# Performance work log

Hardware: AMD Instinct MI355X
Metric: run time of the kernel (lower is better)

The kernel has to match this reference:

```python
import jax, jax.numpy as jnp
import numpy as np

S = 4096            # num tokens (single causal sequence)
HID = 1024          # hidden_size
NH = 16             # num query heads
NKV = 4             # num kv heads
HD = 64             # head_dim
THETA = 10000.0
Q_SIZE = NH * HD
KV_SIZE = NKV * HD


def setup_inputs() -> dict:
    key = jax.random.key(0)
    k1, k2, k3 = jax.random.split(key, 3)
    return {
        "positions": jnp.arange(S, dtype=jnp.int32),
        "hidden_states": jax.random.normal(k1, (S, 2 * HID), dtype=jnp.float32),
        "w_qkv": jax.random.normal(k2, (Q_SIZE + 2 * KV_SIZE, 2 * HID), dtype=jnp.float32) * 0.02,
        "w_o": jax.random.normal(k3, (HID, Q_SIZE), dtype=jnp.float32) * 0.02,
    }


def _rope(x, positions):
    # x: [S, H, HD]; neox-style rotate-half RoPE
    half = HD // 2
    inv_freq = 1.0 / (THETA ** (jnp.arange(0, half, dtype=jnp.float32) / half))
    freqs = positions.astype(jnp.float32)[:, None] * inv_freq  # [S, half]
    cos = jnp.cos(freqs)[:, None, :]  # [S, 1, half]
    sin = jnp.sin(freqs)[:, None, :]
    x1, x2 = x[..., :half], x[..., half:]
    return jnp.concatenate([x1 * cos - x2 * sin, x2 * cos + x1 * sin], axis=-1)


def reference(positions, hidden_states, w_qkv, w_o):
    qkv = hidden_states @ w_qkv.T  # [S, Q_SIZE + 2*KV_SIZE]
    q = qkv[:, :Q_SIZE].reshape(S, NH, HD)
    k = qkv[:, Q_SIZE:Q_SIZE + KV_SIZE].reshape(S, NKV, HD)
    v = qkv[:, Q_SIZE + KV_SIZE:].reshape(S, NKV, HD)
    q = _rope(q, positions)
    k = _rope(k, positions)
    # GQA: group query heads over kv heads
    g = NH // NKV
    qg = q.reshape(S, NKV, g, HD)
    scale = HD ** -0.5
    scores = jnp.einsum("qhgd,thd->hgqt", qg, k) * scale  # [NKV, g, S, S]
    causal = positions[:, None] >= positions[None, :]      # [S, S]
    scores = jnp.where(causal[None, None], scores, jnp.finfo(scores.dtype).min)
    probs = jax.nn.softmax(scores, axis=-1)
    o = jnp.einsum("hgqt,thd->qhgd", probs, v).reshape(S, Q_SIZE)
    return o @ w_o.T  # [S, HID]
```

## Files before the change

kernel.cpp:

```cpp
#include <hip/hip_runtime.h>
#include <math.h>

#define S_LEN   4096
#define NHEADS  16
#define NKVH    4
#define HDIM    64
#define QKV_N   1536
#define HID2    2048
#define OUT_N   1024

typedef __attribute__((ext_vector_type(8))) __bf16 bf16x8;
typedef __attribute__((ext_vector_type(4))) __bf16 bf16x4;
typedef __attribute__((ext_vector_type(4))) float  f32x4;
typedef __attribute__((ext_vector_type(16))) float f32x16;
typedef __attribute__((ext_vector_type(4))) unsigned int u32x4;

#define GL_LDS16(gaddr, laddr)                                                  \
  __builtin_amdgcn_global_load_lds(                                             \
      (const __attribute__((address_space(1))) unsigned int*)(gaddr),           \
      (__attribute__((address_space(3))) unsigned int*)(laddr), 16, 0, 0)

__device__ __forceinline__ unsigned cvt_pk_bf16(float lo, float hi) {
  unsigned r;
  asm("v_cvt_pk_bf16_f32 %0, %1, %2" : "=v"(r) : "v"(lo), "v"(hi));
  return r;
}

__global__ __launch_bounds__(256) void cvt_all(const float* __restrict__ hid,
                                               const float* __restrict__ wq,
                                               const float* __restrict__ wo,
                                               __bf16* __restrict__ hid_bf,
                                               __bf16* __restrict__ wq_bf,
                                               __bf16* __restrict__ wo_bf) {
  const int n1 = S_LEN * HID2;
  const int n2 = QKV_N * HID2;
  int i = (blockIdx.x * blockDim.x + threadIdx.x) * 8;
  const float* src; __bf16* dst; int off;
  if (i < n1)           { src = hid; dst = hid_bf; off = i; }
  else if (i < n1 + n2) { src = wq;  dst = wq_bf;  off = i - n1; }
  else                  { src = wo;  dst = wo_bf;  off = i - n1 - n2; }
  float4 a = *(const float4*)(src + off);
  float4 b = *(const float4*)(src + off + 4);
  bf16x8 o = {(__bf16)a.x,(__bf16)a.y,(__bf16)a.z,(__bf16)a.w,
              (__bf16)b.x,(__bf16)b.y,(__bf16)b.z,(__bf16)b.w};
  *(bf16x8*)(dst + off) = o;
}

__global__ __launch_bounds__(256) void rope_table(const int* __restrict__ positions,
                                                  float* __restrict__ ct,
                                                  float* __restrict__ st) {
  int i = blockIdx.x * blockDim.x + threadIdx.x;
  int s = i >> 5, d = i & 31;
  double inv = pow(10000.0, -(double)d / 32.0);
  double fr = (double)positions[s] * inv;
  ct[i] = (float)cos(fr);
  st[i] = (float)sin(fr);
}

template<int BM, bool C_BF16>
__global__ __launch_bounds__(256) void gemm_m97(const __bf16* __restrict__ A,
                                                const __bf16* __restrict__ B,
                                                void* __restrict__ Cp,
                                                int M, int N, int K) {
  constexpr int TM = BM / 32;
  __shared__ __align__(16) __bf16 As[BM * 32];
  __shared__ __align__(16) __bf16 Bs[128 * 32];
  const int tid  = threadIdx.x;
  const int bm   = blockIdx.x, bn = blockIdx.y;
  const int wave = tid >> 6, lane = tid & 63;
  const int quad = lane >> 4, col = lane & 15;
  const int wm = (wave >> 1) * (BM / 2), wn = (wave & 1) * 64;

  const int lrow = lane >> 2, lcol = (lane & 3) * 8;
  const __bf16* Ag = A + (size_t)(bm * BM + wave * (BM / 4) + lrow) * K + lcol;
  const __bf16* Bg = B + (size_t)(bn * 128 + wave * 32 + lrow) * K + lcol;
  __bf16* AsW = As + wave * (BM / 4) * 32;
  __bf16* BsW = Bs + wave * 32 * 32;

  f32x4 acc[TM][4];
#pragma unroll
  for (int i = 0; i < TM; ++i)
#pragma unroll
    for (int j = 0; j < 4; ++j) acc[i][j] = (f32x4){0.f, 0.f, 0.f, 0.f};

  for (int kk = 0; kk < K; kk += 32) {
    __syncthreads();
#pragma unroll
    for (int u = 0; u < BM / 64; ++u)
      GL_LDS16(Ag + kk + (size_t)(u * 16) * K, AsW + u * 16 * 32);
    GL_LDS16(Bg + kk,                  BsW);
    GL_LDS16(Bg + kk + (size_t)16 * K, BsW + 16 * 32);
    __syncthreads();

    bf16x8 a[TM], b[4];
#pragma unroll
    for (int tm = 0; tm < TM; ++tm)
      a[tm] = *(const bf16x8*)&As[(wm + tm * 16 + col) * 32 + quad * 8];
#pragma unroll
    for (int tn = 0; tn < 4; ++tn)
      b[tn] = *(const bf16x8*)&Bs[(wn + tn * 16 + col) * 32 + quad * 8];
#pragma unroll
    for (int tm = 0; tm < TM; ++tm)
#pragma unroll
      for (int tn = 0; tn < 4; ++tn)
        acc[tm][tn] = __builtin_amdgcn_mfma_f32_16x16x32_bf16(a[tm], b[tn], acc[tm][tn], 0, 0, 0);
  }

#pragma unroll
  for (int tm = 0; tm < TM; ++tm)
#pragma unroll
    for (int tn = 0; tn < 4; ++tn) {
      int row = bm * BM + wm + tm * 16 + quad * 4;
      int cg  = bn * 128 + wn + tn * 16 + col;
#pragma unroll
      for (int r = 0; r < 4; ++r) {
        if constexpr (C_BF16)
          ((__bf16*)Cp)[(size_t)(row + r) * N + cg] = (__bf16)acc[tm][tn][r];
        else
          ((float*)Cp)[(size_t)(row + r) * N + cg] = acc[tm][tn][r];
      }
    }
}

__global__ __launch_bounds__(256) void rope_cast(const __bf16* __restrict__ qkv,
                                                 const float* __restrict__ ct,
                                                 const float* __restrict__ st,
                                                 __bf16* __restrict__ qb,
                                                 __bf16* __restrict__ kb) {
  int g = blockIdx.x * blockDim.x + threadIdx.x;
  int d = g & 31;
  int rem = g >> 5;
  int head = rem % 20;
  int s = rem / 20;
  bool isq = head < NHEADS;
  const __bf16* src = qkv + (size_t)s * QKV_N + (isq ? head * 64 : 1024 + (head - 16) * 64);
  float c  = ct[s * 32 + d];
  float sn = st[s * 32 + d];
  float x1 = (float)src[d], x2 = (float)src[d + 32];
  float y1 = x1 * c - x2 * sn;
  float y2 = x2 * c + x1 * sn;
  float scl = isq ? 0.18033688011112042f : 1.0f;
  __bf16* dst = isq ? (qb + (size_t)s * 1024 + head * 64)
                    : (kb + (size_t)s * 256 + (head - 16) * 64);
  dst[d]      = (__bf16)(y1 * scl);
  dst[d + 32] = (__bf16)(y2 * scl);
}

__global__ __launch_bounds__(256) void v_transpose(const __bf16* __restrict__ qkv,
                                                   __bf16* __restrict__ vT) {
  __shared__ __align__(16) __bf16 Ts[64][72];
  const int sb = blockIdx.x, kvh = blockIdx.y, t = threadIdx.x;
  const int r = t >> 2, c16 = (t & 3) * 16;
  const __bf16* src = qkv + (size_t)(sb * 64 + r) * QKV_N + 1280 + kvh * 64 + c16;
  bf16x8 v0 = *(const bf16x8*)src;
  bf16x8 v1 = *(const bf16x8*)(src + 8);
#pragma unroll
  for (int u = 0; u < 8; ++u) {
    Ts[c16 + u][r]     = v0[u];
    Ts[c16 + 8 + u][r] = v1[u];
  }
  __syncthreads();
  __bf16* dst = vT + ((size_t)kvh * 64 + r) * S_LEN + sb * 64 + c16;
  *(bf16x8*)dst       = *(const bf16x8*)&Ts[r][c16];
  *(bf16x8*)(dst + 8) = *(const bf16x8*)&Ts[r][c16 + 8];
}

__global__ __launch_bounds__(256, 4) void attn_split(const __bf16* __restrict__ qg,
                                                     const __bf16* __restrict__ kg,
                                                     const __bf16* __restrict__ vg,
                                                     __bf16* __restrict__ op0,
                                                     __bf16* __restrict__ op1,
                                                     __bf16* __restrict__ op2,
                                                     __bf16* __restrict__ op3,
                                                     float* __restrict__ lp) {
  __shared__ __align__(16) __bf16 lds[18432];
  __bf16* Ks = lds;
  __bf16* Vs = lds + 9216;

  const int tid = threadIdx.x;
  const int h = blockIdx.x;
  const int y = blockIdx.y;
  int qb, c;
  if (y < 8)       { qb = y;                 c = 0; }
  else if (y < 24) { qb = 8  + ((y - 8) >> 1);  c = (y - 8) & 1; }
  else if (y < 48) { qb = 16 + (y - 24) / 3;    c = (y - 24) % 3; }
  else             { qb = 24 + ((y - 48) >> 2); c = (y - 48) & 3; }
  const int n   = 2 * (qb + 1);
  const int nch = (qb >> 3) + 1;
  const int bsz = n / nch, rm = n - bsz * nch;
  const int kt0 = c * bsz + (c < rm ? c : rm);
  const int ktEnd = kt0 + bsz + (c < rm ? 1 : 0);

  const int kvh = h >> 2;
  const int wave = tid >> 6, lane = tid & 63;
  const int r31 = lane & 31, hi = lane >> 5;
  const int hi4 = hi * 4, hi8 = hi * 8;
  const int qbase = qb * 128 + wave * 32;

  {
    const int r = tid >> 1, cc = (tid & 1) * 32;
    const __bf16* src = qg + (size_t)(qb * 128 + r) * 1024 + h * 64 + cc;
    __bf16* dq = lds + r * 72 + cc;
    *(bf16x8*)(dq)      = *(const bf16x8*)(src);
    *(bf16x8*)(dq + 8)  = *(const bf16x8*)(src + 8);
    *(bf16x8*)(dq + 16) = *(const bf16x8*)(src + 16);
    *(bf16x8*)(dq + 24) = *(const bf16x8*)(src + 24);
  }

  const int sr = tid >> 2, sc = (tid & 3) * 16;
  const __bf16* kptr = kg + (size_t)sr * 256 + kvh * 64 + sc;
  const __bf16* vptr = vg + ((size_t)kvh * 64 + sr) * S_LEN + sc;
  bf16x8 kr0 = *(const bf16x8*)(kptr + (size_t)kt0 * 64 * 256);
  bf16x8 kr1 = *(const bf16x8*)(kptr + (size_t)kt0 * 64 * 256 + 8);
  bf16x8 vr0 = *(const bf16x8*)(vptr + (size_t)kt0 * 64);
  bf16x8 vr1 = *(const bf16x8*)(vptr + (size_t)kt0 * 64 + 8);

  __syncthreads();

  bf16x8 qf[4];
#pragma unroll
  for (int dc = 0; dc < 4; ++dc)
    qf[dc] = *(const bf16x8*)&lds[(wave * 32 + r31) * 72 + dc * 16 + hi8];

  __syncthreads();

  f32x16 fz;
#pragma unroll
  for (int g = 0; g < 16; ++g) fz[g] = 0.f;

  f32x16 o[2];
  o[0] = fz; o[1] = fz;
  float lacc = 0.f;

  for (int kt = kt0; kt < ktEnd; ++kt) {
    const int cur = (kt - kt0) & 1;
    {
      __bf16* kd = Ks + cur * 4608 + sr * 72 + sc;
      *(bf16x8*)kd       = kr0;
      *(bf16x8*)(kd + 8) = kr1;
      __bf16* vd = Vs + cur * 4608 + sr * 72 + sc;
      *(bf16x8*)vd       = vr0;
      *(bf16x8*)(vd + 8) = vr1;
    }
    if (kt + 1 < ktEnd) {
      const __bf16* kn = kptr + (size_t)(kt + 1) * 64 * 256;
      const __bf16* vn = vptr + (size_t)(kt + 1) * 64;
      kr0 = *(const bf16x8*)(kn);
      kr1 = *(const bf16x8*)(kn + 8);
      vr0 = *(const bf16x8*)(vn);
      vr1 = *(const bf16x8*)(vn + 8);
    }
    __syncthreads();

    if (kt * 64 > qbase + 31) continue;

    const bool full = (kt * 64 + 63 <= qbase);
    const int thr = qbase + r31 - kt * 64;

    bf16x8 pa[4];
#pragma unroll
    for (int kb = 0; kb < 2; ++kb) {
      bf16x8 kf0 = *(const bf16x8*)&Ks[cur * 4608 + (kb * 32 + r31) * 72 + hi8];
      f32x16 sf = __builtin_amdgcn_mfma_f32_32x32x16_bf16(kf0, qf[0], fz, 0, 0, 0);
#pragma unroll
      for (int dc = 1; dc < 4; ++dc) {
        bf16x8 kf = *(const bf16x8*)&Ks[cur * 4608 + (kb * 32 + r31) * 72 + dc * 16 + hi8];
        sf = __builtin_amdgcn_mfma_f32_32x32x16_bf16(kf, qf[dc], sf, 0, 0, 0);
      }
      float p[16];
#pragma unroll
      for (int g = 0; g < 16; ++g) {
        float e = __builtin_amdgcn_exp2f(sf[g]);
        if (!full) {
          const int krow = kb * 32 + (g & 3) + 8 * (g >> 2) + hi4;
          if (krow > thr) e = 0.f;
        }
        p[g] = e;
      }
#pragma unroll
      for (int m = 0; m < 4; ++m)
        lacc += (p[4 * m] + p[4 * m + 1]) + (p[4 * m + 2] + p[4 * m + 3]);
#pragma unroll
      for (int half = 0; half < 2; ++half) {
        unsigned a0 = cvt_pk_bf16(p[8 * half + 0], p[8 * half + 1]);
        unsigned a1 = cvt_pk_bf16(p[8 * half + 2], p[8 * half + 3]);
        unsigned b0 = cvt_pk_bf16(p[8 * half + 4], p[8 * half + 5]);
        unsigned b1 = cvt_pk_bf16(p[8 * half + 6], p[8 * half + 7]);
        asm("v_permlane32_swap_b32 %0, %1" : "+v"(a0), "+v"(b0));
        asm("v_permlane32_swap_b32 %0, %1" : "+v"(a1), "+v"(b1));
        u32x4 t = {a0, a1, b0, b1};
        pa[kb * 2 + half] = __builtin_bit_cast(bf16x8, t);
      }
    }

#pragma unroll
    for (int dt = 0; dt < 2; ++dt)
#pragma unroll
      for (int kc = 0; kc < 4; ++kc) {
        bf16x8 vf = *(const bf16x8*)&Vs[cur * 4608 + (dt * 32 + r31) * 72 + kc * 16 + hi8];
        o[dt] = __builtin_amdgcn_mfma_f32_32x32x16_bf16(pa[kc], vf, o[dt], 0, 0, 0);
      }
  }

  lacc += __shfl_xor(lacc, 32, 64);
  __syncthreads();
  float* lshw = (float*)lds + wave * 32;
  if (lane < 32) lshw[lane] = lacc;
  asm volatile("s_waitcnt lgkmcnt(0)" ::: "memory");

  __bf16* op = (c == 0) ? op0 : (c == 1) ? op1 : (c == 2) ? op2 : op3;
#pragma unroll
  for (int g = 0; g < 16; ++g) {
    const int rl = (g & 3) + 8 * (g >> 2) + hi4;
    float l = lshw[rl];
    float linv = (l > 0.f) ? 1.f / l : 0.f;
    const size_t row = (size_t)(qb * 128 + wave * 32 + rl);
    op[row * 1024 + h * 64 + r31]      = (__bf16)(o[0][g] * linv);
    op[row * 1024 + h * 64 + 32 + r31] = (__bf16)(o[1][g] * linv);
  }
  if (lane < 32)
    lp[(size_t)(c * S_LEN + qb * 128 + wave * 32 + lane) * NHEADS + h] = lacc;
}

__global__ __launch_bounds__(256) void attn_combine(const __bf16* __restrict__ op0,
                                                    const __bf16* __restrict__ op1,
                                                    const __bf16* __restrict__ op2,
                                                    const __bf16* __restrict__ op3,
                                                    const float* __restrict__ lp,
                                                    __bf16* __restrict__ ob) {
  int i = blockIdx.x * 256 + threadIdx.x;
  int row = i >> 7, c8 = (i & 127) * 8;
  int h = c8 >> 6;
  const int nch = (row >> 10) + 1;
  float l0 = lp[(size_t)row * NHEADS + h];
  float l1 = (nch > 1) ? lp[(size_t)(S_LEN + row) * NHEADS + h] : 0.f;
  float l2 = (nch > 2) ? lp[(size_t)(2 * S_LEN + row) * NHEADS + h] : 0.f;
  float l3 = (nch > 3) ? lp[(size_t)(3 * S_LEN + row) * NHEADS + h] : 0.f;
  float inv = 1.f / (l0 + l1 + l2 + l3);
  float acc[8];
  bf16x8 a = *(const bf16x8*)(op0 + (size_t)row * 1024 + c8);
#pragma unroll
  for (int u = 0; u < 8; ++u) acc[u] = (float)a[u] * l0;
  if (nch > 1) {
    bf16x8 b = *(const bf16x8*)(op1 + (size_t)row * 1024 + c8);
#pragma unroll
    for (int u = 0; u < 8; ++u) acc[u] += (float)b[u] * l1;
  }
  if (nch > 2) {
    bf16x8 b = *(const bf16x8*)(op2 + (size_t)row * 1024 + c8);
#pragma unroll
    for (int u = 0; u < 8; ++u) acc[u] += (float)b[u] * l2;
  }
  if (nch > 3) {
    bf16x8 b = *(const bf16x8*)(op3 + (size_t)row * 1024 + c8);
#pragma unroll
    for (int u = 0; u < 8; ++u) acc[u] += (float)b[u] * l3;
  }
  bf16x8 o;
#pragma unroll
  for (int u = 0; u < 8; ++u) o[u] = (__bf16)(acc[u] * inv);
  *(bf16x8*)(ob + (size_t)row * 1024 + c8) = o;
}

extern "C" void kernel_launch(void* const* d_in, const int* in_sizes, int n_in,
                              void* d_out, int out_size, void* d_ws, size_t ws_size,
                              hipStream_t stream) {
  const int*   positions = (const int*)d_in[0];
  const float* hidden    = (const float*)d_in[1];
  const float* w_qkv     = (const float*)d_in[2];
  const float* w_o       = (const float*)d_in[3];
  float* out = (float*)d_out;

  char* ws = (char*)d_ws;
  __bf16* qkv_bf  = (__bf16*)ws;
  __bf16* Opart0  = (__bf16*)ws;
  __bf16* attn_bf = (__bf16*)ws;
  float*  lpart   = (float*)(ws + 8388608);
  __bf16* hid_bf  = (__bf16*)(ws + 12582912);
  __bf16* q_bf    = (__bf16*)(ws + 12582912);
  __bf16* k_bf    = (__bf16*)(ws + 20971520);
  __bf16* vT      = (__bf16*)(ws + 23068672);
  float*  ct      = (float*)(ws + 29360128);
  float*  st      = (float*)(ws + 29884416);
  __bf16* wq_bf   = (__bf16*)(ws + 30408704);
  __bf16* Opart1  = (__bf16*)(ws + 30408704);
  __bf16* wo_bf   = (__bf16*)(ws + 38797312);
  __bf16* Opart2  = (__bf16*)d_out;
  __bf16* Opart3  = (__bf16*)((char*)d_out + 8388608);

  cvt_all<<<(S_LEN * HID2 + QKV_N * HID2 + OUT_N * OUT_N) / 8 / 256, 256, 0, stream>>>(
      hidden, w_qkv, w_o, hid_bf, wq_bf, wo_bf);
  rope_table<<<S_LEN * 32 / 256, 256, 0, stream>>>(positions, ct, st);

  gemm_m97<64, true><<<dim3(S_LEN / 64, QKV_N / 128), 256, 0, stream>>>(
      hid_bf, wq_bf, qkv_bf, S_LEN, QKV_N, HID2);

  rope_cast<<<(S_LEN * 20 * 32) / 256, 256, 0, stream>>>(qkv_bf, ct, st, q_bf, k_bf);
  v_transpose<<<dim3(S_LEN / 64, NKVH), 256, 0, stream>>>(qkv_bf, vT);

  attn_split<<<dim3(NHEADS, 80), 256, 0, stream>>>(q_bf, k_bf, vT,
                                                   Opart0, Opart1, Opart2, Opart3,
                                                   lpart);
  attn_combine<<<S_LEN * 128 / 256, 256, 0, stream>>>(Opart0, Opart1, Opart2, Opart3,
                                                      lpart, attn_bf);

  gemm_m97<64, false><<<dim3(S_LEN / 64, OUT_N / 128), 256, 0, stream>>>(
      attn_bf, wo_bf, out, S_LEN, OUT_N, OUT_N);
}
```

Before: 242.7 us.

## Merge small prep kernels, vectorize RoPE, and schedule heavy attention blocks first

Folds the RoPE table computation into the conversion kernel and merges rope_cast with the V transpose into one launch, cutting two kernel launches. RoPE now has one thread handle a full 64-wide head row with 16-byte vector loads and stores instead of scalar per-element access. The attention grid's y index is reversed so the blocks with the longest causal spans launch first, which should reduce tail imbalance. Per-thread register use in the RoPE path goes up.

After: 238.1 us. Within noise of the previous version (-1.9%).

```diff
diff --git a/kernel.cpp b/kernel.cpp
--- a/kernel.cpp
+++ b/kernel.cpp
@@ -26,35 +26,37 @@
   return r;
 }
 
+#define CVT_BLOCKS 6144
 __global__ __launch_bounds__(256) void cvt_all(const float* __restrict__ hid,
                                                const float* __restrict__ wq,
                                                const float* __restrict__ wo,
+                                               const int* __restrict__ positions,
                                                __bf16* __restrict__ hid_bf,
                                                __bf16* __restrict__ wq_bf,
-                                               __bf16* __restrict__ wo_bf) {
-  const int n1 = S_LEN * HID2;
-  const int n2 = QKV_N * HID2;
-  int i = (blockIdx.x * blockDim.x + threadIdx.x) * 8;
-  const float* src; __bf16* dst; int off;
-  if (i < n1)           { src = hid; dst = hid_bf; off = i; }
-  else if (i < n1 + n2) { src = wq;  dst = wq_bf;  off = i - n1; }
-  else                  { src = wo;  dst = wo_bf;  off = i - n1 - n2; }
-  float4 a = *(const float4*)(src + off);
-  float4 b = *(const float4*)(src + off + 4);
-  bf16x8 o = {(__bf16)a.x,(__bf16)a.y,(__bf16)a.z,(__bf16)a.w,
-              (__bf16)b.x,(__bf16)b.y,(__bf16)b.z,(__bf16)b.w};
-  *(bf16x8*)(dst + off) = o;
-}
-
-__global__ __launch_bounds__(256) void rope_table(const int* __restrict__ positions,
-                                                  float* __restrict__ ct,
-                                                  float* __restrict__ st) {
-  int i = blockIdx.x * blockDim.x + threadIdx.x;
-  int s = i >> 5, d = i & 31;
-  double inv = pow(10000.0, -(double)d / 32.0);
-  double fr = (double)positions[s] * inv;
-  ct[i] = (float)cos(fr);
-  st[i] = (float)sin(fr);
+                                               __bf16* __restrict__ wo_bf,
+                                               float* __restrict__ ct,
+                                               float* __restrict__ st) {
+  if (blockIdx.x < CVT_BLOCKS) {
+    const int n1 = S_LEN * HID2;
+    const int n2 = QKV_N * HID2;
+    int i = (blockIdx.x * blockDim.x + threadIdx.x) * 8;
+    const float* src; __bf16* dst; int off;
+    if (i < n1)           { src = hid; dst = hid_bf; off = i; }
+    else if (i < n1 + n2) { src = wq;  dst = wq_bf;  off = i - n1; }
+    else                  { src = wo;  dst = wo_bf;  off = i - n1 - n2; }
+    float4 a = *(const float4*)(src + off);
+    float4 b = *(const float4*)(src + off + 4);
+    bf16x8 o = {(__bf16)a.x,(__bf16)a.y,(__bf16)a.z,(__bf16)a.w,
+                (__bf16)b.x,(__bf16)b.y,(__bf16)b.z,(__bf16)b.w};
+    *(bf16x8*)(dst + off) = o;
+  } else {
+    int i = (blockIdx.x - CVT_BLOCKS) * blockDim.x + threadIdx.x;
+    int s = i >> 5, d = i & 31;
+    double inv = pow(10000.0, -(double)d / 32.0);
+    double fr = (double)positions[s] * inv;
+    ct[i] = (float)cos(fr);
+    st[i] = (float)sin(fr);
+  }
 }
 
 template<int BM, bool C_BF16>
@@ -122,47 +124,61 @@
     }
 }
 
-__global__ __launch_bounds__(256) void rope_cast(const __bf16* __restrict__ qkv,
-                                                 const float* __restrict__ ct,
-                                                 const float* __restrict__ st,
-                                                 __bf16* __restrict__ qb,
-                                                 __bf16* __restrict__ kb) {
-  int g = blockIdx.x * blockDim.x + threadIdx.x;
-  int d = g & 31;
-  int rem = g >> 5;
-  int head = rem % 20;
-  int s = rem / 20;
-  bool isq = head < NHEADS;
-  const __bf16* src = qkv + (size_t)s * QKV_N + (isq ? head * 64 : 1024 + (head - 16) * 64);
-  float c  = ct[s * 32 + d];
-  float sn = st[s * 32 + d];
-  float x1 = (float)src[d], x2 = (float)src[d + 32];
-  float y1 = x1 * c - x2 * sn;
-  float y2 = x2 * c + x1 * sn;
-  float scl = isq ? 0.18033688011112042f : 1.0f;
-  __bf16* dst = isq ? (qb + (size_t)s * 1024 + head * 64)
-                    : (kb + (size_t)s * 256 + (head - 16) * 64);
-  dst[d]      = (__bf16)(y1 * scl);
-  dst[d + 32] = (__bf16)(y2 * scl);
-}
-
-__global__ __launch_bounds__(256) void v_transpose(const __bf16* __restrict__ qkv,
-                                                   __bf16* __restrict__ vT) {
-  __shared__ __align__(16) __bf16 Ts[64][72];
-  const int sb = blockIdx.x, kvh = blockIdx.y, t = threadIdx.x;
-  const int r = t >> 2, c16 = (t & 3) * 16;
-  const __bf16* src = qkv + (size_t)(sb * 64 + r) * QKV_N + 1280 + kvh * 64 + c16;
-  bf16x8 v0 = *(const bf16x8*)src;
-  bf16x8 v1 = *(const bf16x8*)(src + 8);
-#pragma unroll
-  for (int u = 0; u < 8; ++u) {
-    Ts[c16 + u][r]     = v0[u];
-    Ts[c16 + 8 + u][r] = v1[u];
-  }
-  __syncthreads();
-  __bf16* dst = vT + ((size_t)kvh * 64 + r) * S_LEN + sb * 64 + c16;
-  *(bf16x8*)dst       = *(const bf16x8*)&Ts[r][c16];
-  *(bf16x8*)(dst + 8) = *(const bf16x8*)&Ts[r][c16 + 8];
+#define RC_BLOCKS 320
+__global__ __launch_bounds__(256) void rope_cast_vt(const __bf16* __restrict__ qkv,
+                                                    const float* __restrict__ ct,
+                                                    const float* __restrict__ st,
+                                                    __bf16* __restrict__ qb,
+                                                    __bf16* __restrict__ kb,
+                                                    __bf16* __restrict__ vT) {
+  if (blockIdx.x < RC_BLOCKS) {
+    int g = blockIdx.x * 256 + threadIdx.x;
+    int head = g % 20, s = g / 20;
+    bool isq = head < NHEADS;
+    const __bf16* src = qkv + (size_t)s * QKV_N +
+                        (isq ? head * 64 : 1024 + (head - 16) * 64);
+    bf16x8 x[8];
+#pragma unroll
+    for (int u = 0; u < 8; ++u) x[u] = *(const bf16x8*)(src + u * 8);
+    float cc[32], ss[32];
+#pragma unroll
+    for (int u = 0; u < 8; ++u) {
+      float4 c4 = *(const float4*)(ct + s * 32 + u * 4);
+      float4 s4 = *(const float4*)(st + s * 32 + u * 4);
+      cc[4*u] = c4.x; cc[4*u+1] = c4.y; cc[4*u+2] = c4.z; cc[4*u+3] = c4.w;
+      ss[4*u] = s4.x; ss[4*u+1] = s4.y; ss[4*u+2] = s4.z; ss[4*u+3] = s4.w;
+    }
+    const float scl = isq ? 0.18033688011112042f : 1.0f;
+    bf16x8 o[8];
+#pragma unroll
+    for (int d = 0; d < 32; ++d) {
+      float x1 = (float)x[d >> 3][d & 7];
+      float x2 = (float)x[4 + (d >> 3)][d & 7];
+      o[d >> 3][d & 7]       = (__bf16)((x1 * cc[d] - x2 * ss[d]) * scl);
+      o[4 + (d >> 3)][d & 7] = (__bf16)((x2 * cc[d] + x1 * ss[d]) * scl);
+    }
+    __bf16* dst = isq ? (qb + (size_t)s * 1024 + head * 64)
+                      : (kb + (size_t)s * 256 + (head - 16) * 64);
+#pragma unroll
+    for (int u = 0; u < 8; ++u) *(bf16x8*)(dst + u * 8) = o[u];
+  } else {
+    __shared__ __align__(16) __bf16 Ts[64][72];
+    const int idx = blockIdx.x - RC_BLOCKS;
+    const int sb = idx & 63, kvh = idx >> 6, t = threadIdx.x;
+    const int r = t >> 2, c16 = (t & 3) * 16;
+    const __bf16* src = qkv + (size_t)(sb * 64 + r) * QKV_N + 1280 + kvh * 64 + c16;
+    bf16x8 v0 = *(const bf16x8*)src;
+    bf16x8 v1 = *(const bf16x8*)(src + 8);
+#pragma unroll
+    for (int u = 0; u < 8; ++u) {
+      Ts[c16 + u][r]     = v0[u];
+      Ts[c16 + 8 + u][r] = v1[u];
+    }
+    __syncthreads();
+    __bf16* dst = vT + ((size_t)kvh * 64 + r) * S_LEN + sb * 64 + c16;
+    *(bf16x8*)dst       = *(const bf16x8*)&Ts[r][c16];
+    *(bf16x8*)(dst + 8) = *(const bf16x8*)&Ts[r][c16 + 8];
+  }
 }
 
 __global__ __launch_bounds__(256, 4) void attn_split(const __bf16* __restrict__ qg,
@@ -179,7 +195,7 @@
 
   const int tid = threadIdx.x;
   const int h = blockIdx.x;
-  const int y = blockIdx.y;
+  const int y = 79 - (int)blockIdx.y;
   int qb, c;
   if (y < 8)       { qb = y;                 c = 0; }
   else if (y < 24) { qb = 8  + ((y - 8) >> 1);  c = (y - 8) & 1; }
@@ -388,15 +404,14 @@
   __bf16* Opart2  = (__bf16*)d_out;
   __bf16* Opart3  = (__bf16*)((char*)d_out + 8388608);
 
-  cvt_all<<<(S_LEN * HID2 + QKV_N * HID2 + OUT_N * OUT_N) / 8 / 256, 256, 0, stream>>>(
-      hidden, w_qkv, w_o, hid_bf, wq_bf, wo_bf);
-  rope_table<<<S_LEN * 32 / 256, 256, 0, stream>>>(positions, ct, st);
+  cvt_all<<<CVT_BLOCKS + S_LEN * 32 / 256, 256, 0, stream>>>(
+      hidden, w_qkv, w_o, positions, hid_bf, wq_bf, wo_bf, ct, st);
 
   gemm_m97<64, true><<<dim3(S_LEN / 64, QKV_N / 128), 256, 0, stream>>>(
       hid_bf, wq_bf, qkv_bf, S_LEN, QKV_N, HID2);
 
-  rope_cast<<<(S_LEN * 20 * 32) / 256, 256, 0, stream>>>(qkv_bf, ct, st, q_bf, k_bf);
-  v_transpose<<<dim3(S_LEN / 64, NKVH), 256, 0, stream>>>(qkv_bf, vT);
+  rope_cast_vt<<<RC_BLOCKS + S_LEN / 64 * NKVH, 256, 0, stream>>>(
+      qkv_bf, ct, st, q_bf, k_bf, vT);
 
   attn_split<<<dim3(NHEADS, 80), 256, 0, stream>>>(q_bf, k_bf, vT,
                                                    Opart0, Opart1, Opart2, Opart3,
```
